# Performance work log

Hardware: AMD Instinct MI355X
Metric: run time of the kernel (lower is better)

Reference implementation:

```python
import jax, jax.numpy as jnp
import numpy as np

GRID_SHAPE = (256, 256)  # SOM lattice dims -> M = 65536 nodes, ndim = 2
D = 32                   # input feature dim
B = 2048                 # batch size


def _make_grid_flat():
    # tf.meshgrid(indexing='ij') stacked on last axis, flattened to [1, M, ndim]
    mesh = np.stack(np.meshgrid(*[np.arange(s) for s in GRID_SHAPE], indexing='ij'), axis=-1)
    g = mesh.reshape(1, -1, len(GRID_SHAPE)).astype(np.float32)
    # faithful to source: per-axis mean (reduce_mean axis=1), GLOBAL std (reduce_std, no axis)
    g = (g - g.mean(axis=1, keepdims=True)) / g.std()
    return jnp.asarray(g)


def setup_inputs() -> dict:
    key = jax.random.key(0)
    k1, k2 = jax.random.split(key)
    grid_flat = _make_grid_flat()                                  # [1, M, 2]
    M = grid_flat.shape[1]
    w = jax.random.normal(k1, (1, M, D), dtype=jnp.float32)        # codebook (non-trainable in source)
    x = jax.random.normal(k2, (B, D), dtype=jnp.float32)
    return {"x": x, "grid_flat": grid_flat, "w": w}


def reference(x, grid_flat, w):
    # squared L2 distance from each input to every codebook vector.
    # computed here without materializing the [B, M, D] broadcast.
    wm = w[0]  # [M, D]
    d2 = (jnp.sum(x * x, axis=1, keepdims=True)
          - 2.0 * (x @ wm.T)
          + jnp.sum(wm * wm, axis=1)[None, :])  # [B, M]
    # source: top_k(-|d2|, k=1); d2 >= 0 so abs is identity, kept for fidelity
    _, idx = jax.lax.top_k(-jnp.abs(d2), 1)  # idx: [B, 1]
    bmu = grid_flat[0][idx[:, 0]]            # gather winning grid coords -> [B, 2]
    return bmu
```

## Files before the change

### kernel.cpp

```cpp
#include <hip/hip_runtime.h>
#include <stdint.h>

#define D       32
#define B       2048
#define M       65536
#define STRIPS  1024
#define CHUNKS  4
#define CHCOLS  (B / CHUNKS)
#define NTILES  (CHCOLS / 16)
#define SGROUPS 32
#define SPERG   (STRIPS / SGROUPS)
#define MARGIN  0.15f

typedef _Float16 half8  __attribute__((ext_vector_type(8)));
typedef _Float16 half4v __attribute__((ext_vector_type(4)));
typedef float    floatx4 __attribute__((ext_vector_type(4)));


__device__ __forceinline__ uint32_t f32_sortable(float f) {
    uint32_t u = __float_as_uint(f);
    u ^= (uint32_t)((int32_t)u >> 31) | 0x80000000u;
    return u;
}
__device__ __forceinline__ float sort_decode(uint32_t u) {
    uint32_t m = (u & 0x80000000u) ? (u ^ 0x80000000u) : ~u;
    return __uint_as_float(m);
}

__global__ void som_prep_kernel(const float* __restrict__ x,
                                _Float16* __restrict__ xh) {
    int i = (blockIdx.x * 256 + threadIdx.x) * 4;
    float4 v = *(const float4*)(x + i);
    half4v h;
    h[0] = (_Float16)v.x; h[1] = (_Float16)v.y;
    h[2] = (_Float16)v.z; h[3] = (_Float16)v.w;
    *(half4v*)(xh + i) = h;
}

__global__ __launch_bounds__(256, 4)
void som_screen_kernel(const float* __restrict__ w,
                       const _Float16* __restrict__ x_hi,
                       uint32_t* __restrict__ pmax) {
    const int s    = blockIdx.x;
    const int wv   = threadIdx.x >> 6;
    const int lane = threadIdx.x & 63;
    const int q    = lane >> 4;
    const int j    = lane & 15;

    half8 a_hi[4];
    float nrm[4];
#pragma unroll
    for (int t = 0; t < 4; t++) {
        const float* wp = w + (size_t)(s * 64 + t * 16 + j) * D + q * 8;
        float4 f0 = ((const float4*)wp)[0];
        float4 f1 = ((const float4*)wp)[1];
        float f[8] = {f0.x, f0.y, f0.z, f0.w, f1.x, f1.y, f1.z, f1.w};
        float sq = 0.0f;
#pragma unroll
        for (int k = 0; k < 8; k++) {
            a_hi[t][k] = (_Float16)f[k];
            sq = fmaf(f[k], f[k], sq);
        }
        sq += __shfl_xor(sq, 16);
        sq += __shfl_xor(sq, 32);
        nrm[t] = sq;
    }

    floatx4 init[4];
#pragma unroll
    for (int t = 0; t < 4; t++)
#pragma unroll
        for (int r = 0; r < 4; r++)
            init[t][r] = -0.5f * __shfl(nrm[t], q * 4 + r);

    uint32_t* pm = pmax + (size_t)s * B;

#pragma unroll 2
    for (int it = 0; it < NTILES; it++) {
        const int col = wv * CHCOLS + it * 16 + j;
        const half8 bh = *(const half8*)(x_hi + (size_t)col * D + q * 8);

        floatx4 acc[4];
#pragma unroll
        for (int t = 0; t < 4; t++)
            acc[t] = __builtin_amdgcn_mfma_f32_16x16x32_f16(a_hi[t], bh, init[t], 0, 0, 0);

        float b0 = fmaxf(fmaxf(acc[0][0], acc[0][1]), fmaxf(acc[0][2], acc[0][3]));
        float b1 = fmaxf(fmaxf(acc[1][0], acc[1][1]), fmaxf(acc[1][2], acc[1][3]));
        float b2 = fmaxf(fmaxf(acc[2][0], acc[2][1]), fmaxf(acc[2][2], acc[2][3]));
        float b3 = fmaxf(fmaxf(acc[3][0], acc[3][1]), fmaxf(acc[3][2], acc[3][3]));
        float best = fmaxf(fmaxf(b0, b1), fmaxf(b2, b3));

        best = fmaxf(best, __shfl_xor(best, 16));
        best = fmaxf(best, __shfl_xor(best, 32));

        if (lane < 16) pm[col] = f32_sortable(best);
    }
}

__global__ void som_reduce1_kernel(const uint32_t* __restrict__ pmax,
                                   uint64_t* __restrict__ s2) {
    const int col = blockIdx.x * 256 + threadIdx.x;
    const int sg  = blockIdx.y;
    uint32_t best = pmax[(size_t)(sg * SPERG) * B + col];
    int bstrip = sg * SPERG;
#pragma unroll 8
    for (int t = 1; t < SPERG; t++) {
        uint32_t u = pmax[(size_t)(sg * SPERG + t) * B + col];
        if (u > best) { best = u; bstrip = sg * SPERG + t; }
    }
    s2[(size_t)sg * B + col] = ((uint64_t)best << 32) | (uint32_t)(~(uint32_t)bstrip);
}

__device__ __forceinline__ void rescore_strip(int strip, int lane,
                                              const float* __restrict__ w,
                                              const float* xr,
                                              uint64_t& best) {
    const int row = strip * 64 + lane;
    const float* wr = w + (size_t)row * D;
    float4 w0 = ((const float4*)wr)[0];
    float4 w1 = ((const float4*)wr)[1];
    float4 w2 = ((const float4*)wr)[2];
    float4 w3 = ((const float4*)wr)[3];
    float4 w4 = ((const float4*)wr)[4];
    float4 w5 = ((const float4*)wr)[5];
    float4 w6 = ((const float4*)wr)[6];
    float4 w7 = ((const float4*)wr)[7];
    const float wf[32] = {w0.x,w0.y,w0.z,w0.w, w1.x,w1.y,w1.z,w1.w,
                          w2.x,w2.y,w2.z,w2.w, w3.x,w3.y,w3.z,w3.w,
                          w4.x,w4.y,w4.z,w4.w, w5.x,w5.y,w5.z,w5.w,
                          w6.x,w6.y,w6.z,w6.w, w7.x,w7.y,w7.z,w7.w};
    float acc = 0.0f, nn = 0.0f;
#pragma unroll
    for (int i = 0; i < D; i++) {
        acc = fmaf(xr[i], wf[i], acc);
        nn  = fmaf(wf[i], wf[i], nn);
    }
    const float score = acc - 0.5f * nn;
    const uint64_t key = ((uint64_t)f32_sortable(score) << 32)
                       | (uint32_t)(~(uint32_t)row);
    if (key > best) best = key;
}

__global__ __launch_bounds__(256)
void som_final_kernel(const uint64_t* __restrict__ s2,
                      const uint32_t* __restrict__ pmax,
                      const float* __restrict__ x,
                      const float* __restrict__ w,
                      const float* __restrict__ grid_flat,
                      float* __restrict__ out) {
    const int wv   = threadIdx.x >> 6;
    const int lane = threadIdx.x & 63;
    const int col  = blockIdx.x * 4 + wv;

    uint64_t k = (lane < SGROUPS) ? s2[(size_t)lane * B + col] : 0ull;
    uint64_t kmax = k;
    {
        uint64_t o;
        o = (uint64_t)__shfl_xor((long long)kmax,  1); if (o > kmax) kmax = o;
        o = (uint64_t)__shfl_xor((long long)kmax,  2); if (o > kmax) kmax = o;
        o = (uint64_t)__shfl_xor((long long)kmax,  4); if (o > kmax) kmax = o;
        o = (uint64_t)__shfl_xor((long long)kmax,  8); if (o > kmax) kmax = o;
        o = (uint64_t)__shfl_xor((long long)kmax, 16); if (o > kmax) kmax = o;
        o = (uint64_t)__shfl_xor((long long)kmax, 32); if (o > kmax) kmax = o;
    }
    const float    v1       = sort_decode((uint32_t)(kmax >> 32));
    const uint32_t thresh_u = f32_sortable(v1 - MARGIN);

    float xr[D];
    const float4* xp = (const float4*)(x + (size_t)col * D);
#pragma unroll
    for (int i = 0; i < D / 4; i++) {
        float4 v = xp[i];
        xr[4*i+0] = v.x; xr[4*i+1] = v.y; xr[4*i+2] = v.z; xr[4*i+3] = v.w;
    }

    uint64_t best = 0;
    unsigned long long gmask =
        __ballot((lane < SGROUPS) && ((uint32_t)(k >> 32) >= thresh_u));
    while (gmask) {
        const int g = __ffsll(gmask) - 1;
        gmask &= gmask - 1;
        uint32_t u = 0;
        if (lane < SPERG) u = pmax[(size_t)(g * SPERG + lane) * B + col];
        unsigned long long smask = __ballot((lane < SPERG) && (u >= thresh_u));
        while (smask) {
            const int sl = __ffsll(smask) - 1;
            smask &= smask - 1;
            rescore_strip(g * SPERG + sl, lane, w, xr, best);
        }
    }

    {
        uint64_t o;
        o = (uint64_t)__shfl_xor((long long)best,  1); if (o > best) best = o;
        o = (uint64_t)__shfl_xor((long long)best,  2); if (o > best) best = o;
        o = (uint64_t)__shfl_xor((long long)best,  4); if (o > best) best = o;
        o = (uint64_t)__shfl_xor((long long)best,  8); if (o > best) best = o;
        o = (uint64_t)__shfl_xor((long long)best, 16); if (o > best) best = o;
        o = (uint64_t)__shfl_xor((long long)best, 32); if (o > best) best = o;
    }
    if (lane == 0) {
        const uint32_t idx = ~(uint32_t)best;
        ((float2*)out)[col] = ((const float2*)grid_flat)[idx];
    }
}

#define MTILES  128
#define MTILE   (M / MTILES)
#define BTILE   256

__global__ void som_wnorm_kernel(const float* __restrict__ w,
                                 float* __restrict__ wnorm) {
    int t   = blockIdx.x * blockDim.x + threadIdx.x;
    int row = t >> 2;
    int j   = t & 3;
    const float4* p = (const float4*)(w + (size_t)row * D) + j * 2;
    float4 a = p[0];
    float4 b4 = p[1];
    float s = a.x * a.x + a.y * a.y + a.z * a.z + a.w * a.w
            + b4.x * b4.x + b4.y * b4.y + b4.z * b4.z + b4.w * b4.w;
    s += __shfl_xor(s, 1);
    s += __shfl_xor(s, 2);
    if (j == 0) wnorm[row] = 0.5f * s;
}

__global__ __launch_bounds__(BTILE, 8)
void som_score_kernel(const float* __restrict__ x,
                      const float* __restrict__ w,
                      const float* __restrict__ wnorm,
                      float* __restrict__ pscore,
                      int*   __restrict__ pidx) {
    const int bt = blockIdx.x;
    const int mt = blockIdx.y;
    const int b  = bt * BTILE + threadIdx.x;

    float xr[D];
    const float4* xp = (const float4*)(x + (size_t)b * D);
#pragma unroll
    for (int i = 0; i < D / 4; i++) {
        float4 v = xp[i];
        xr[4 * i + 0] = v.x; xr[4 * i + 1] = v.y;
        xr[4 * i + 2] = v.z; xr[4 * i + 3] = v.w;
    }

    const int m0 = mt * MTILE;
    float best = -3.0e38f;
    int   bidx = m0;
#pragma unroll 2
    for (int mm = 0; mm < MTILE; mm++) {
        const int m = m0 + mm;
        const float* __restrict__ wr = w + (size_t)m * D;
        float acc = 0.0f;
#pragma unroll
        for (int i = 0; i < D; i++) acc = fmaf(xr[i], wr[i], acc);
        const float score = acc - wnorm[m];
        if (score > best) { best = score; bidx = m; }
    }
    pscore[(size_t)b * MTILES + mt] = best;
    pidx  [(size_t)b * MTILES + mt] = bidx;
}

__global__ void som_reduce_kernel(const float* __restrict__ pscore,
                                  const int*   __restrict__ pidx,
                                  const float* __restrict__ grid_flat,
                                  float* __restrict__ out) {
    const int b = blockIdx.x * blockDim.x + threadIdx.x;
    const float* ps = pscore + (size_t)b * MTILES;
    const int*   pi = pidx   + (size_t)b * MTILES;
    float best = -3.0e38f;
    int   bidx = 0x7fffffff;
#pragma unroll 4
    for (int t = 0; t < MTILES; t++) {
        const float s  = ps[t];
        const int   id = pi[t];
        if (s > best || (s == best && id < bidx)) { best = s; bidx = id; }
    }
    ((float2*)out)[b] = ((const float2*)grid_flat)[bidx];
}

extern "C" void kernel_launch(void* const* d_in, const int* in_sizes, int n_in,
                              void* d_out, int out_size, void* d_ws, size_t ws_size,
                              hipStream_t stream) {
    const float* x         = (const float*)d_in[0];
    const float* grid_flat = (const float*)d_in[1];
    const float* w         = (const float*)d_in[2];
    float* out = (float*)d_out;

    char* ws = (char*)d_ws;
    const size_t XH_OFF = 0;
    const size_t PM_OFF = XH_OFF + (size_t)B * D * sizeof(_Float16);
    const size_t S2_OFF = PM_OFF + (size_t)STRIPS * B * sizeof(uint32_t);
    const size_t NEED   = S2_OFF + (size_t)SGROUPS * B * sizeof(uint64_t);

    if (ws_size >= NEED) {
        _Float16* x_hi = (_Float16*)(ws + XH_OFF);
        uint32_t* pmax = (uint32_t*)(ws + PM_OFF);
        uint64_t* s2   = (uint64_t*)(ws + S2_OFF);

        som_prep_kernel<<<(B * D / 4) / 256, 256, 0, stream>>>(x, x_hi);
        som_screen_kernel<<<STRIPS, 256, 0, stream>>>(w, x_hi, pmax);
        som_reduce1_kernel<<<dim3(B / 256, SGROUPS), 256, 0, stream>>>(pmax, s2);
        som_final_kernel<<<B / 4, 256, 0, stream>>>(s2, pmax, x, w, grid_flat, out);
    } else {
        float* wnorm  = (float*)d_ws;
        float* pscore = wnorm + M;
        int*   pidx   = (int*)(pscore + (size_t)B * MTILES);

        som_wnorm_kernel<<<(M * 4) / 256, 256, 0, stream>>>(w, wnorm);
        dim3 grid1(B / BTILE, MTILES);
        som_score_kernel<<<grid1, BTILE, 0, stream>>>(x, w, wnorm, pscore, pidx);
        som_reduce_kernel<<<B / 256, 256, 0, stream>>>(pscore, pidx, grid_flat, out);
    }
}
```

Measured before the change: 99.01 us.

## Fuse strip-group max reduction into screen kernel via atomicMax and drop reduce pass

The screen kernel now handles two strips per block and folds the per-group maximum directly into a gmax buffer with atomicMax. The prep kernel zeroes that buffer, which removes the separate reduce1 kernel launch and its full re-read of pmax. The final kernel now reads 32-bit group maxima instead of 64-bit keys carrying strip indices. In exchange it adds global atomics (16 blocks contend per group column) and halves the number of screen blocks while raising register use per block.

```diff
diff --git a/kernel.cpp b/kernel.cpp
--- a/kernel.cpp
+++ b/kernel.cpp
@@ -28,88 +28,94 @@
 }
 
 __global__ void som_prep_kernel(const float* __restrict__ x,
-                                _Float16* __restrict__ xh) {
-    int i = (blockIdx.x * 256 + threadIdx.x) * 4;
+                                _Float16* __restrict__ xh,
+                                uint32_t* __restrict__ gmax) {
+    const int tid = blockIdx.x * 256 + threadIdx.x;
+    const int i   = tid * 4;
     float4 v = *(const float4*)(x + i);
     half4v h;
     h[0] = (_Float16)v.x; h[1] = (_Float16)v.y;
     h[2] = (_Float16)v.z; h[3] = (_Float16)v.w;
     *(half4v*)(xh + i) = h;
-}
-
-__global__ __launch_bounds__(256, 4)
+    ((uint4*)gmax)[tid] = make_uint4(0u, 0u, 0u, 0u);
+}
+
+__global__ __launch_bounds__(256, 2)
 void som_screen_kernel(const float* __restrict__ w,
                        const _Float16* __restrict__ x_hi,
-                       uint32_t* __restrict__ pmax) {
-    const int s    = blockIdx.x;
+                       uint32_t* __restrict__ pmax,
+                       uint32_t* __restrict__ gmax) {
+    const int sA   = blockIdx.x * 2;
     const int wv   = threadIdx.x >> 6;
     const int lane = threadIdx.x & 63;
     const int q    = lane >> 4;
     const int j    = lane & 15;
 
-    half8 a_hi[4];
-    float nrm[4];
-#pragma unroll
-    for (int t = 0; t < 4; t++) {
-        const float* wp = w + (size_t)(s * 64 + t * 16 + j) * D + q * 8;
-        float4 f0 = ((const float4*)wp)[0];
-        float4 f1 = ((const float4*)wp)[1];
-        float f[8] = {f0.x, f0.y, f0.z, f0.w, f1.x, f1.y, f1.z, f1.w};
-        float sq = 0.0f;
-#pragma unroll
-        for (int k = 0; k < 8; k++) {
-            a_hi[t][k] = (_Float16)f[k];
-            sq = fmaf(f[k], f[k], sq);
+    half8   a_hi[2][4];
+    floatx4 init[2][4];
+#pragma unroll
+    for (int p = 0; p < 2; p++) {
+        float nrm[4];
+#pragma unroll
+        for (int t = 0; t < 4; t++) {
+            const float* wp = w + (size_t)((sA + p) * 64 + t * 16 + j) * D + q * 8;
+            float4 f0 = ((const float4*)wp)[0];
+            float4 f1 = ((const float4*)wp)[1];
+            float f[8] = {f0.x, f0.y, f0.z, f0.w, f1.x, f1.y, f1.z, f1.w};
+            float sq = 0.0f;
+#pragma unroll
+            for (int k = 0; k < 8; k++) {
+                a_hi[p][t][k] = (_Float16)f[k];
+                sq = fmaf(f[k], f[k], sq);
+            }
+            sq += __shfl_xor(sq, 16);
+            sq += __shfl_xor(sq, 32);
+            nrm[t] = sq;
         }
-        sq += __shfl_xor(sq, 16);
-        sq += __shfl_xor(sq, 32);
-        nrm[t] = sq;
-    }
-
-    floatx4 init[4];
-#pragma unroll
-    for (int t = 0; t < 4; t++)
-#pragma unroll
-        for (int r = 0; r < 4; r++)
-            init[t][r] = -0.5f * __shfl(nrm[t], q * 4 + r);
-
-    uint32_t* pm = pmax + (size_t)s * B;
-
-#pragma unroll 2
+#pragma unroll
+        for (int t = 0; t < 4; t++)
+#pragma unroll
+            for (int r = 0; r < 4; r++)
+                init[p][t][r] = -0.5f * __shfl(nrm[t], q * 4 + r);
+    }
+
+    uint32_t* pm0 = pmax + (size_t)sA * B;
+    uint32_t* pm1 = pmax + (size_t)(sA + 1) * B;
+    uint32_t* gm  = gmax + (size_t)(sA >> 5) * B;
+
     for (int it = 0; it < NTILES; it++) {
         const int col = wv * CHCOLS + it * 16 + j;
         const half8 bh = *(const half8*)(x_hi + (size_t)col * D + q * 8);
 
-        floatx4 acc[4];
-#pragma unroll
-        for (int t = 0; t < 4; t++)
-            acc[t] = __builtin_amdgcn_mfma_f32_16x16x32_f16(a_hi[t], bh, init[t], 0, 0, 0);
-
-        float b0 = fmaxf(fmaxf(acc[0][0], acc[0][1]), fmaxf(acc[0][2], acc[0][3]));
-        float b1 = fmaxf(fmaxf(acc[1][0], acc[1][1]), fmaxf(acc[1][2], acc[1][3]));
-        float b2 = fmaxf(fmaxf(acc[2][0], acc[2][1]), fmaxf(acc[2][2], acc[2][3]));
-        float b3 = fmaxf(fmaxf(acc[3][0], acc[3][1]), fmaxf(acc[3][2], acc[3][3]));
-        float best = fmaxf(fmaxf(b0, b1), fmaxf(b2, b3));
-
-        best = fmaxf(best, __shfl_xor(best, 16));
-        best = fmaxf(best, __shfl_xor(best, 32));
-
-        if (lane < 16) pm[col] = f32_sortable(best);
-    }
-}
-
-__global__ void som_reduce1_kernel(const uint32_t* __restrict__ pmax,
-                                   uint64_t* __restrict__ s2) {
-    const int col = blockIdx.x * 256 + threadIdx.x;
-    const int sg  = blockIdx.y;
-    uint32_t best = pmax[(size_t)(sg * SPERG) * B + col];
-    int bstrip = sg * SPERG;
-#pragma unroll 8
-    for (int t = 1; t < SPERG; t++) {
-        uint32_t u = pmax[(size_t)(sg * SPERG + t) * B + col];
-        if (u > best) { best = u; bstrip = sg * SPERG + t; }
-    }
-    s2[(size_t)sg * B + col] = ((uint64_t)best << 32) | (uint32_t)(~(uint32_t)bstrip);
+        floatx4 acc[2][4];
+#pragma unroll
+        for (int p = 0; p < 2; p++)
+#pragma unroll
+            for (int t = 0; t < 4; t++)
+                acc[p][t] = __builtin_amdgcn_mfma_f32_16x16x32_f16(
+                    a_hi[p][t], bh, init[p][t], 0, 0, 0);
+
+        float best[2];
+#pragma unroll
+        for (int p = 0; p < 2; p++) {
+            float b0 = fmaxf(fmaxf(acc[p][0][0], acc[p][0][1]), fmaxf(acc[p][0][2], acc[p][0][3]));
+            float b1 = fmaxf(fmaxf(acc[p][1][0], acc[p][1][1]), fmaxf(acc[p][1][2], acc[p][1][3]));
+            float b2 = fmaxf(fmaxf(acc[p][2][0], acc[p][2][1]), fmaxf(acc[p][2][2], acc[p][2][3]));
+            float b3 = fmaxf(fmaxf(acc[p][3][0], acc[p][3][1]), fmaxf(acc[p][3][2], acc[p][3][3]));
+            float bb = fmaxf(fmaxf(b0, b1), fmaxf(b2, b3));
+            bb = fmaxf(bb, __shfl_xor(bb, 16));
+            bb = fmaxf(bb, __shfl_xor(bb, 32));
+            best[p] = bb;
+        }
+
+        if (lane < 16) {
+            const uint32_t u0 = f32_sortable(best[0]);
+            const uint32_t u1 = f32_sortable(best[1]);
+            pm0[col] = u0;
+            pm1[col] = u1;
+            atomicMax(&gm[col], u0 > u1 ? u0 : u1);
+        }
+    }
 }
 
 __device__ __forceinline__ void rescore_strip(int strip, int lane,
@@ -143,7 +149,7 @@
 }
 
 __global__ __launch_bounds__(256)
-void som_final_kernel(const uint64_t* __restrict__ s2,
+void som_final_kernel(const uint32_t* __restrict__ gmax,
                       const uint32_t* __restrict__ pmax,
                       const float* __restrict__ x,
                       const float* __restrict__ w,
@@ -153,19 +159,15 @@
     const int lane = threadIdx.x & 63;
     const int col  = blockIdx.x * 4 + wv;
 
-    uint64_t k = (lane < SGROUPS) ? s2[(size_t)lane * B + col] : 0ull;
-    uint64_t kmax = k;
-    {
-        uint64_t o;
-        o = (uint64_t)__shfl_xor((long long)kmax,  1); if (o > kmax) kmax = o;
-        o = (uint64_t)__shfl_xor((long long)kmax,  2); if (o > kmax) kmax = o;
-        o = (uint64_t)__shfl_xor((long long)kmax,  4); if (o > kmax) kmax = o;
-        o = (uint64_t)__shfl_xor((long long)kmax,  8); if (o > kmax) kmax = o;
-        o = (uint64_t)__shfl_xor((long long)kmax, 16); if (o > kmax) kmax = o;
-        o = (uint64_t)__shfl_xor((long long)kmax, 32); if (o > kmax) kmax = o;
-    }
-    const float    v1       = sort_decode((uint32_t)(kmax >> 32));
-    const uint32_t thresh_u = f32_sortable(v1 - MARGIN);
+    const uint32_t g = (lane < SGROUPS) ? gmax[(size_t)lane * B + col] : 0u;
+    uint32_t vmax = g;
+    vmax = max(vmax, (uint32_t)__shfl_xor((int)vmax,  1));
+    vmax = max(vmax, (uint32_t)__shfl_xor((int)vmax,  2));
+    vmax = max(vmax, (uint32_t)__shfl_xor((int)vmax,  4));
+    vmax = max(vmax, (uint32_t)__shfl_xor((int)vmax,  8));
+    vmax = max(vmax, (uint32_t)__shfl_xor((int)vmax, 16));
+    vmax = max(vmax, (uint32_t)__shfl_xor((int)vmax, 32));
+    const uint32_t thresh_u = f32_sortable(sort_decode(vmax) - MARGIN);
 
     float xr[D];
     const float4* xp = (const float4*)(x + (size_t)col * D);
@@ -176,18 +178,17 @@
     }
 
     uint64_t best = 0;
-    unsigned long long gmask =
-        __ballot((lane < SGROUPS) && ((uint32_t)(k >> 32) >= thresh_u));
+    unsigned long long gmask = __ballot((lane < SGROUPS) && (g >= thresh_u));
     while (gmask) {
-        const int g = __ffsll(gmask) - 1;
+        const int gi = __ffsll(gmask) - 1;
         gmask &= gmask - 1;
         uint32_t u = 0;
-        if (lane < SPERG) u = pmax[(size_t)(g * SPERG + lane) * B + col];
+        if (lane < SPERG) u = pmax[(size_t)(gi * SPERG + lane) * B + col];
         unsigned long long smask = __ballot((lane < SPERG) && (u >= thresh_u));
         while (smask) {
             const int sl = __ffsll(smask) - 1;
             smask &= smask - 1;
-            rescore_strip(g * SPERG + sl, lane, w, xr, best);
+            rescore_strip(gi * SPERG + sl, lane, w, xr, best);
         }
     }
 
@@ -290,18 +291,17 @@
     char* ws = (char*)d_ws;
     const size_t XH_OFF = 0;
     const size_t PM_OFF = XH_OFF + (size_t)B * D * sizeof(_Float16);
-    const size_t S2_OFF = PM_OFF + (size_t)STRIPS * B * sizeof(uint32_t);
-    const size_t NEED   = S2_OFF + (size_t)SGROUPS * B * sizeof(uint64_t);
+    const size_t GM_OFF = PM_OFF + (size_t)STRIPS * B * sizeof(uint32_t);
+    const size_t NEED   = GM_OFF + (size_t)SGROUPS * B * sizeof(uint32_t);
 
     if (ws_size >= NEED) {
         _Float16* x_hi = (_Float16*)(ws + XH_OFF);
         uint32_t* pmax = (uint32_t*)(ws + PM_OFF);
-        uint64_t* s2   = (uint64_t*)(ws + S2_OFF);
-
-        som_prep_kernel<<<(B * D / 4) / 256, 256, 0, stream>>>(x, x_hi);
-        som_screen_kernel<<<STRIPS, 256, 0, stream>>>(w, x_hi, pmax);
-        som_reduce1_kernel<<<dim3(B / 256, SGROUPS), 256, 0, stream>>>(pmax, s2);
-        som_final_kernel<<<B / 4, 256, 0, stream>>>(s2, pmax, x, w, grid_flat, out);
+        uint32_t* gmax = (uint32_t*)(ws + GM_OFF);
+
+        som_prep_kernel<<<(B * D / 4) / 256, 256, 0, stream>>>(x, x_hi, gmax);
+        som_screen_kernel<<<STRIPS / 2, 256, 0, stream>>>(w, x_hi, pmax, gmax);
+        som_final_kernel<<<B / 4, 256, 0, stream>>>(gmax, pmax, x, w, grid_flat, out);
     } else {
         float* wnorm  = (float*)d_ws;
         float* pscore = wnorm + M;
```

Measured after the change: 101.7 us. 1.03x slower.
